# Kernel optimization log

Measured on AMD Instinct MI355X. Metric: run time of the kernel, lower is better.

The kernel has to match this reference:

```python
import jax, jax.numpy as jnp
import numpy as np

M, N, NUM_ITER, BATCH = 512, 2048, 16, 4096


def setup_inputs() -> dict:
    key = jax.random.key(0)
    k_y, k_D, k_thr = jax.random.split(key, 3)
    # Dictionary D (== A in the module), column-scaled like a sensing matrix
    D = np.asarray(jax.random.normal(k_D, (M, N), dtype=jnp.float32)) / np.sqrt(M)
    # W = inv(D D^T) D, then normalize columns so w_i . d_i == 1 (ALISTA analytic weight)
    W = np.linalg.inv(D @ D.T) @ D
    W = W / np.sum(W * D, axis=0, keepdims=True)
    y = jax.random.normal(k_y, (BATCH, M), dtype=jnp.float32)
    thr = jax.random.uniform(k_thr, (NUM_ITER,), dtype=jnp.float32) * 0.1  # positive thresholds
    step = jnp.ones((NUM_ITER,), dtype=jnp.float32)
    return {"y": y, "A": jnp.asarray(D), "W": jnp.asarray(W), "thr": thr, "step": step}


def reference(y, A, W, thr, step):
    # y: [B, m]; A, W: [m, n]; thr, step: [numIter]
    B = y.shape[0]
    n = A.shape[1]

    def body(d, ts):
        t, s = ts
        r = d @ A.T - y                      # [B, m]  == (A @ d.T - y.T).T
        z = d - s * (r @ W)                  # [B, n]  == (W.T @ r.T).T
        d_new = jnp.sign(z) * jnp.maximum(jnp.abs(z) - t, 0.0)  # soft threshold
        return d_new, d_new

    d0 = jnp.zeros((B, n), dtype=y.dtype)
    _, xs = jax.lax.scan(body, d0, (thr, step))
    return xs  # [numIter, B, n]: all intermediate iterates, like the returned list x
```

## Files before the change

### kernel.cpp

```cpp
#include <hip/hip_runtime.h>


#define NDIM 2048
#define MDIM 512
#define BATCHN 4096
#define NITER 16

#define BM2 256
#define BN2 128
#define BK3 64

typedef _Float16 f16;
typedef f16 f16x8 __attribute__((ext_vector_type(8)));
typedef float f32x4 __attribute__((ext_vector_type(4)));

__device__ __forceinline__ void gload_lds16(const void* g, void* lds) {
  __builtin_amdgcn_global_load_lds(
      (const __attribute__((address_space(1))) unsigned int*)g,
      (__attribute__((address_space(3))) unsigned int*)lds, 16, 0, 0);
}

template <int EPI, int NK>
__global__ __launch_bounds__(512, 2) void gemm_phased(
    const f16* __restrict__ Aop, const f16* __restrict__ Bop,
    const f16* __restrict__ Ds, const f16* __restrict__ Ch,
    const float* __restrict__ thr, const float* __restrict__ step, int it,
    float sigma, float inv_sigma, float inv_sigma_next,
    float* __restrict__ outIter, f16* __restrict__ DsNext,
    f16* __restrict__ outH)
{
  constexpr int K = NK * BK3;
  __shared__ __align__(16) f16 ldsAll[3 * BM2 * BK3 + 3 * BN2 * BK3];
  f16* ldsA = ldsAll;
  f16* ldsB = ldsAll + 3 * BM2 * BK3;

  const int tid = threadIdx.x;
  const int w = tid >> 6, l = tid & 63;
  const int ks = w & 1;
  const int wn = (w >> 1) & 1;
  const int wm = w >> 2;
  const int h = l >> 4;

  const int bid = blockIdx.x;
  const int cpx = (int)(gridDim.x >> 3);
  const int wgid = (bid & 7) * cpx + (bid >> 3);
  const int rowTile = (wgid >> 4) * BM2;
  const int colTile = (wgid & 15) * BN2;

  const f16* Abase = Aop + (size_t)rowTile * K;
  const f16* Bbase = Bop + (size_t)colTile * K;

  auto stageA = [&](int buf, int t, int r) {
    int row = r * 64 + (tid >> 3);
    int gsw = ((tid & 7) ^ (row & 7)) << 4;
    gload_lds16((const char*)(Abase + (size_t)row * K + t * BK3) + gsw,
                (char*)ldsA + buf * 32768 + r * 8192 + w * 1024);
  };
  auto stageB = [&](int buf, int t, int r) {
    int row = r * 64 + (tid >> 3);
    int gsw = ((tid & 7) ^ (row & 7)) << 4;
    gload_lds16((const char*)(Bbase + (size_t)row * K + t * BK3) + gsw,
                (char*)ldsB + buf * 16384 + r * 8192 + w * 1024);
  };

#define READ_A4(bR, mOfs, af)                                                   \
  {                                                                             \
    const f16* bA_ = ldsA + (bR) * 16384;                                       \
    const int c_ = ks * 4 + h;                                                  \
    _Pragma("unroll")                                                           \
    for (int m = 0; m < 4; ++m) {                                               \
      int row = wm * 128 + ((mOfs) + m) * 16 + (l & 15);                        \
      af[m] = *(const f16x8*)(bA_ + row * 64 + ((c_ ^ (row & 7)) << 3));        \
    }                                                                           \
  }
#define READ_B4(bR, bf)                                                         \
  {                                                                             \
    const f16* bB_ = ldsB + (bR) * 8192;                                        \
    const int c_ = ks * 4 + h;                                                  \
    _Pragma("unroll")                                                           \
    for (int n = 0; n < 4; ++n) {                                               \
      int row = wn * 64 + n * 16 + (l & 15);                                    \
      bf[n] = *(const f16x8*)(bB_ + row * 64 + ((c_ ^ (row & 7)) << 3));        \
    }                                                                           \
  }

#define MFMA16(accOfs, af, bf)                                                  \
  __builtin_amdgcn_s_setprio(1);                                                \
  _Pragma("unroll")                                                             \
  for (int m = 0; m < 4; ++m)                                                   \
    _Pragma("unroll")                                                           \
    for (int n = 0; n < 4; ++n)                                                 \
      acc[(accOfs) + m][n] = __builtin_amdgcn_mfma_f32_16x16x32_f16(            \
          af[m], bf[n], acc[(accOfs) + m][n], 0, 0, 0);                         \
  __builtin_amdgcn_s_setprio(0);

  f32x4 acc[8][4] = {};
  f16x8 afE[4], afO[4], bf[4];

#pragma unroll
  for (int r = 0; r < 4; ++r) stageA(0, 0, r);
#pragma unroll
  for (int r = 0; r < 2; ++r) stageB(0, 0, r);
#pragma unroll
  for (int r = 0; r < 4; ++r) stageA(1, 1, r);
#pragma unroll
  for (int r = 0; r < 2; ++r) stageB(1, 1, r);
  asm volatile("s_waitcnt vmcnt(6)" ::: "memory");
  __builtin_amdgcn_s_barrier();
  __builtin_amdgcn_sched_barrier(0);

  int bR = 0;
  int bS = 2;

  for (int t = 0; t < NK; ++t) {
    const bool pf = (t + 2 < NK);

    READ_A4(bR, 0, afE);
    READ_B4(bR, bf);
    READ_A4(bR, 4, afO);
    if (pf) {
      stageA(bS, t + 2, 0); stageA(bS, t + 2, 1);
      stageA(bS, t + 2, 2); stageA(bS, t + 2, 3);
      stageB(bS, t + 2, 0); stageB(bS, t + 2, 1);
    }
    __builtin_amdgcn_sched_barrier(0);
    __builtin_amdgcn_s_barrier();
    asm volatile("s_waitcnt lgkmcnt(4)" ::: "memory");
    __builtin_amdgcn_sched_barrier(0);
    MFMA16(0, afE, bf);
    asm volatile("s_waitcnt lgkmcnt(0)" ::: "memory");
    __builtin_amdgcn_sched_barrier(0);
    MFMA16(4, afO, bf);
    if (pf) asm volatile("s_waitcnt vmcnt(6)" ::: "memory");
    else    asm volatile("s_waitcnt vmcnt(0)" ::: "memory");
    __builtin_amdgcn_s_barrier();
    __builtin_amdgcn_sched_barrier(0);

    bR = (bR == 2) ? 0 : bR + 1;
    bS = (bS == 2) ? 0 : bS + 1;
  }

  float* xb = (float*)ldsAll;
  const int p = w >> 1;
  const size_t sbase = (size_t)p * 8192 + (size_t)ks * 4096;
  const size_t rbase = (size_t)p * 8192 + (size_t)(ks ^ 1) * 4096;
  if (ks == 0) {
#pragma unroll
    for (int m4 = 0; m4 < 4; ++m4)
#pragma unroll
      for (int n = 0; n < 4; ++n)
        *(f32x4*)(xb + sbase + l * 64 + (((m4 * 4 + n) ^ (l & 15)) << 2)) = acc[4 + m4][n];
  } else {
#pragma unroll
    for (int m4 = 0; m4 < 4; ++m4)
#pragma unroll
      for (int n = 0; n < 4; ++n)
        *(f32x4*)(xb + sbase + l * 64 + (((m4 * 4 + n) ^ (l & 15)) << 2)) = acc[m4][n];
  }
  __syncthreads();
  if (ks == 0) {
#pragma unroll
    for (int m4 = 0; m4 < 4; ++m4)
#pragma unroll
      for (int n = 0; n < 4; ++n)
        acc[m4][n] += *(const f32x4*)(xb + rbase + l * 64 + (((m4 * 4 + n) ^ (l & 15)) << 2));
  } else {
#pragma unroll
    for (int m4 = 0; m4 < 4; ++m4)
#pragma unroll
      for (int n = 0; n < 4; ++n)
        acc[4 + m4][n] += *(const f32x4*)(xb + rbase + l * 64 + (((m4 * 4 + n) ^ (l & 15)) << 2));
  }

  const int baseRow = rowTile + wm * 128 + ks * 64 + (h << 2);
  const int baseCol = colTile + wn * 64 + (l & 15);
  float s = 0.f, tt = 0.f;
  size_t itOff = 0;
  if (EPI >= 1) {
    s = step[it];
    tt = thr[it];
    itOff = (size_t)it * (size_t)BATCHN * NDIM;
  }
#define EPILOG(ACCOFS)                                                          \
  _Pragma("unroll")                                                             \
  for (int m4 = 0; m4 < 4; ++m4)                                                \
    _Pragma("unroll")                                                           \
    for (int n = 0; n < 4; ++n)                                                 \
      _Pragma("unroll")                                                         \
      for (int r = 0; r < 4; ++r) {                                             \
        int row = baseRow + m4 * 16 + r;                                        \
        int col = baseCol + n * 16;                                             \
        size_t g = (size_t)row * NDIM + col;                                    \
        float v = acc[(ACCOFS) + m4][n][r];                                     \
        if (EPI == 0) {                                                         \
          outH[g] = (f16)v;                                                     \
        } else if (EPI == 1) {                                                  \
          outH[g] = (f16)v;                                                     \
          float z = s * v;                                                      \
          float az = __builtin_fabsf(z) - tt;                                   \
          float dn = az > 0.f ? (z > 0.f ? az : -az) : 0.f;                     \
          outIter[g] = dn;                                                      \
          DsNext[g] = (f16)dn;                                                  \
        } else {                                                                \
          float ds = (float)Ds[g];                                              \
          float cv = (float)Ch[g];                                              \
          float z = sigma * (ds - s * (v - cv * inv_sigma));                    \
          float az = __builtin_fabsf(z) - tt;                                   \
          float dn = az > 0.f ? (z > 0.f ? az : -az) : 0.f;                     \
          outIter[itOff + g] = dn;                                              \
          DsNext[g] = (f16)(dn * inv_sigma_next);                               \
        }                                                                       \
      }
  if (ks == 0) { EPILOG(0) } else { EPILOG(4) }
#undef EPILOG
#undef READ_A4
#undef READ_B4
#undef MFMA16
}

__global__ __launch_bounds__(256) void preprep(
    const float* __restrict__ A, const float* __restrict__ W,
    const float* __restrict__ y,
    f16* __restrict__ Ath, f16* __restrict__ Wth, f16* __restrict__ yh)
{
  int b = blockIdx.x;
  int t = threadIdx.x;
  if (b < 512) {
    const float* in = (b < 256) ? A : W;
    f16* oh = (b < 256) ? Ath : Wth;
    int bb = b & 255;
    __shared__ float tile[64][65];
    int tr = t >> 6;
    int tc = t & 63;
    int r0 = (bb >> 5) * 64;
    int c0 = (bb & 31) * 64;
#pragma unroll
    for (int i = 0; i < 16; ++i) {
      int r = i * 4 + tr;
      tile[r][tc] = in[(size_t)(r0 + r) * NDIM + c0 + tc];
    }
    __syncthreads();
#pragma unroll
    for (int i = 0; i < 16; ++i) {
      int r = i * 4 + tr;
      oh[(size_t)(c0 + r) * MDIM + r0 + tc] = (f16)tile[tc][r];
    }
  } else {
    size_t base = (size_t)(b - 512) * 256 * 32 + t;
#pragma unroll
    for (int i = 0; i < 32; ++i)
      yh[base + i * 256] = (f16)y[base + i * 256];
  }
}

extern "C" void kernel_launch(void* const* d_in, const int* in_sizes, int n_in,
                              void* d_out, int out_size, void* d_ws, size_t ws_size,
                              hipStream_t stream)
{
  const float* y    = (const float*)d_in[0];
  const float* A    = (const float*)d_in[1];
  const float* W    = (const float*)d_in[2];
  const float* thr  = (const float*)d_in[3];
  const float* step = (const float*)d_in[4];
  float* out = (float*)d_out;
  char* ws = (char*)d_ws;

  f16* Pht = (f16*)(ws + 0);
  f16* Ch  = (f16*)(ws + (8ull  << 20));
  f16* DsA = (f16*)(ws + (24ull << 20));
  f16* DsB = (f16*)(ws + (40ull << 20));
  f16* Wth = (f16*)(ws + (40ull << 20));
  f16* Ath = (f16*)(ws + (42ull << 20));
  f16* yh  = (f16*)(ws + (44ull << 20));

  preprep<<<dim3(768), 256, 0, stream>>>(A, W, y, Ath, Wth, yh);

  gemm_phased<0, MDIM / BK3><<<dim3(128), 512, 0, stream>>>(
      Wth, Ath, nullptr, nullptr, thr, step, 0,
      0.f, 0.f, 0.f, nullptr, nullptr, Pht);

  gemm_phased<1, MDIM / BK3><<<dim3(256), 512, 0, stream>>>(
      yh, Wth, nullptr, nullptr, thr, step, 0,
      0.f, 0.f, 1.0f, out, DsA, Ch);

  f16* cur = DsA;
  f16* nxt = DsB;
  float sigma = 1.0f;
  for (int it = 1; it < NITER; ++it) {
    gemm_phased<2, NDIM / BK3><<<dim3(256), 512, 0, stream>>>(
        cur, Pht, cur, Ch, thr, step, it,
        sigma, 1.0f / sigma, 0.25f / sigma, out, nxt, nullptr);
    sigma *= 4.0f;
    f16* tmp = cur; cur = nxt; nxt = tmp;
  }
}
```

Baseline: 745.0 us.

## Fold identity into Gram matrix, split K-step pipeline into two half-phases, prefetch C early

The precomputed Gram operand now stores (I - W^T A), so with unit step the update becomes z = sigma*v + c and the epilogue no longer reads the previous iterate D from global memory. The non-unit-step path still reads it. Ch values are loaded into registers before the cross-wave LDS reduction to hide their latency. The main loop now reads only half the A fragments at a time and issues the global-to-LDS prefetch in two halves, with an extra barrier. This saves fragment registers but adds synchronization, and the identity subtraction in fp16 may change rounding.

```diff
diff --git a/kernel.cpp b/kernel.cpp
--- a/kernel.cpp
+++ b/kernel.cpp
@@ -95,7 +95,7 @@
   __builtin_amdgcn_s_setprio(0);
 
   f32x4 acc[8][4] = {};
-  f16x8 afE[4], afO[4], bf[4];
+  f16x8 af[4], bf[4];
 
 #pragma unroll
   for (int r = 0; r < 4; ++r) stageA(0, 0, r);
@@ -115,22 +115,21 @@
   for (int t = 0; t < NK; ++t) {
     const bool pf = (t + 2 < NK);
 
-    READ_A4(bR, 0, afE);
+    READ_A4(bR, 0, af);
     READ_B4(bR, bf);
-    READ_A4(bR, 4, afO);
-    if (pf) {
-      stageA(bS, t + 2, 0); stageA(bS, t + 2, 1);
-      stageA(bS, t + 2, 2); stageA(bS, t + 2, 3);
-      stageB(bS, t + 2, 0); stageB(bS, t + 2, 1);
-    }
-    __builtin_amdgcn_sched_barrier(0);
+    if (pf) { stageA(bS, t + 2, 0); stageA(bS, t + 2, 1); stageB(bS, t + 2, 0); }
     __builtin_amdgcn_s_barrier();
-    asm volatile("s_waitcnt lgkmcnt(4)" ::: "memory");
-    __builtin_amdgcn_sched_barrier(0);
-    MFMA16(0, afE, bf);
     asm volatile("s_waitcnt lgkmcnt(0)" ::: "memory");
     __builtin_amdgcn_sched_barrier(0);
-    MFMA16(4, afO, bf);
+    MFMA16(0, af, bf);
+    __builtin_amdgcn_s_barrier();
+
+    READ_A4(bR, 4, af);
+    if (pf) { stageA(bS, t + 2, 2); stageA(bS, t + 2, 3); stageB(bS, t + 2, 1); }
+    __builtin_amdgcn_s_barrier();
+    asm volatile("s_waitcnt lgkmcnt(0)" ::: "memory");
+    __builtin_amdgcn_sched_barrier(0);
+    MFMA16(4, af, bf);
     if (pf) asm volatile("s_waitcnt vmcnt(6)" ::: "memory");
     else    asm volatile("s_waitcnt vmcnt(0)" ::: "memory");
     __builtin_amdgcn_s_barrier();
@@ -138,6 +137,20 @@
 
     bR = (bR == 2) ? 0 : bR + 1;
     bS = (bS == 2) ? 0 : bS + 1;
+  }
+
+  const int baseRow = rowTile + wm * 128 + ks * 64 + (h << 2);
+  const int baseCol = colTile + wn * 64 + (l & 15);
+
+  f16 chv[4][4][4];
+  if (EPI == 2) {
+#pragma unroll
+    for (int m4 = 0; m4 < 4; ++m4)
+#pragma unroll
+      for (int n = 0; n < 4; ++n)
+#pragma unroll
+        for (int r = 0; r < 4; ++r)
+          chv[m4][n][r] = Ch[(size_t)(baseRow + m4 * 16 + r) * NDIM + baseCol + n * 16];
   }
 
   float* xb = (float*)ldsAll;
@@ -172,14 +185,14 @@
         acc[4 + m4][n] += *(const f32x4*)(xb + rbase + l * 64 + (((m4 * 4 + n) ^ (l & 15)) << 2));
   }
 
-  const int baseRow = rowTile + wm * 128 + ks * 64 + (h << 2);
-  const int baseCol = colTile + wn * 64 + (l & 15);
   float s = 0.f, tt = 0.f;
   size_t itOff = 0;
+  bool sUnit = true;
   if (EPI >= 1) {
     s = step[it];
     tt = thr[it];
     itOff = (size_t)it * (size_t)BATCHN * NDIM;
+    sUnit = (s == 1.0f);
   }
 #define EPILOG(ACCOFS)                                                          \
   _Pragma("unroll")                                                             \
@@ -193,7 +206,7 @@
         size_t g = (size_t)row * NDIM + col;                                    \
         float v = acc[(ACCOFS) + m4][n][r];                                     \
         if (EPI == 0) {                                                         \
-          outH[g] = (f16)v;                                                     \
+          outH[g] = (f16)((row == col ? 1.0f : 0.0f) - v);                      \
         } else if (EPI == 1) {                                                  \
           outH[g] = (f16)v;                                                     \
           float z = s * v;                                                      \
@@ -202,9 +215,11 @@
           outIter[g] = dn;                                                      \
           DsNext[g] = (f16)dn;                                                  \
         } else {                                                                \
-          float ds = (float)Ds[g];                                              \
-          float cv = (float)Ch[g];                                              \
-          float z = sigma * (ds - s * (v - cv * inv_sigma));                    \
+           \
+          float cv = (float)chv[m4][n][r];                                      \
+          float z;                                                              \
+          if (sUnit) z = sigma * v + cv;                                        \
+          else       z = sigma * (s * v + (1.f - s) * (float)Ds[g]) + s * cv;   \
           float az = __builtin_fabsf(z) - tt;                                   \
           float dn = az > 0.f ? (z > 0.f ? az : -az) : 0.f;                     \
           outIter[itOff + g] = dn;                                              \
@@ -265,7 +280,7 @@
   float* out = (float*)d_out;
   char* ws = (char*)d_ws;
 
-  f16* Pht = (f16*)(ws + 0);
+  f16* Qht = (f16*)(ws + 0);
   f16* Ch  = (f16*)(ws + (8ull  << 20));
   f16* DsA = (f16*)(ws + (24ull << 20));
   f16* DsB = (f16*)(ws + (40ull << 20));
@@ -277,7 +292,7 @@
 
   gemm_phased<0, MDIM / BK3><<<dim3(128), 512, 0, stream>>>(
       Wth, Ath, nullptr, nullptr, thr, step, 0,
-      0.f, 0.f, 0.f, nullptr, nullptr, Pht);
+      0.f, 0.f, 0.f, nullptr, nullptr, Qht);
 
   gemm_phased<1, MDIM / BK3><<<dim3(256), 512, 0, stream>>>(
       yh, Wth, nullptr, nullptr, thr, step, 0,
@@ -288,7 +303,7 @@
   float sigma = 1.0f;
   for (int it = 1; it < NITER; ++it) {
     gemm_phased<2, NDIM / BK3><<<dim3(256), 512, 0, stream>>>(
-        cur, Pht, cur, Ch, thr, step, it,
+        cur, Qht, cur, Ch, thr, step, it,
         sigma, 1.0f / sigma, 0.25f / sigma, out, nxt, nullptr);
     sigma *= 4.0f;
     f16* tmp = cur; cur = nxt; nxt = tmp;
```

Result: slower. 986.6 us (+32.4%).
